# Optimization experiments

Hardware: AMD Instinct MI355X
Metric: run time of the kernel (lower is better)

Reference implementation:

```python
import jax, jax.numpy as jnp
import numpy as np

N = 5000        # n_stocks (nodes)
F = 128         # n_features
H = 4           # attention heads
C = 32          # hidden_size per head
HC = H * C      # GAT output dim = GRU input dim
GH = 256        # gru_hidden_size
E = 320000      # directed edges (before self-loops)
NEG_SLOPE = 0.2 # GATv2Conv default leaky_relu slope


def setup_inputs() -> dict:
    key = jax.random.key(0)
    ks = jax.random.split(key, 16)
    s = 0.05
    return {
        "x": jax.random.normal(ks[0], (N, F), dtype=jnp.float32),
        "edge_index": jax.random.randint(ks[1], (2, E), 0, N, dtype=jnp.int64),
        # GATv2Conv params (lin_l, lin_r with bias, attention vector, output bias)
        "W_l": jax.random.normal(ks[2], (F, HC), dtype=jnp.float32) * s,
        "b_l": jax.random.normal(ks[3], (HC,), dtype=jnp.float32) * s,
        "W_r": jax.random.normal(ks[4], (F, HC), dtype=jnp.float32) * s,
        "b_r": jax.random.normal(ks[5], (HC,), dtype=jnp.float32) * s,
        "att": jax.random.normal(ks[6], (H, C), dtype=jnp.float32) * s,
        "gat_bias": jax.random.normal(ks[7], (HC,), dtype=jnp.float32) * s,
        # GRU params (single layer, PyTorch gate order r,z,n)
        "W_ih": jax.random.normal(ks[8], (3 * GH, HC), dtype=jnp.float32) * s,
        "W_hh": jax.random.normal(ks[9], (3 * GH, GH), dtype=jnp.float32) * s,
        "b_ih": jax.random.normal(ks[10], (3 * GH,), dtype=jnp.float32) * s,
        "b_hh": jax.random.normal(ks[11], (3 * GH,), dtype=jnp.float32) * s,
        # policy head + log_std param
        "Wp": jax.random.normal(ks[12], (N, GH), dtype=jnp.float32) * s,
        "bp": jax.random.normal(ks[13], (N,), dtype=jnp.float32) * s,
        "log_std": jnp.zeros((N,), dtype=jnp.float32),
    }


def reference(x, edge_index, W_l, b_l, W_r, b_r, att, gat_bias,
              W_ih, W_hh, b_ih, b_hh, Wp, bp, log_std):
    # --- GATv2Conv (add_self_loops=True, concat heads, eval mode -> no dropout) ---
    loop = jnp.arange(N, dtype=edge_index.dtype)
    src = jnp.concatenate([edge_index[0], loop])  # message source j
    dst = jnp.concatenate([edge_index[1], loop])  # message target i

    xl = (x @ W_l + b_l).reshape(N, H, C)  # source-side transform
    xr = (x @ W_r + b_r).reshape(N, H, C)  # target-side transform

    m = xl[src] + xr[dst]                                  # [Etot, H, C]
    e = jnp.einsum('ehc,hc->eh', jax.nn.leaky_relu(m, NEG_SLOPE), att)

    # segment softmax over incoming edges per target node
    emax = jax.ops.segment_max(e, dst, num_segments=N)      # [N, H]
    ex = jnp.exp(e - emax[dst])
    denom = jax.ops.segment_sum(ex, dst, num_segments=N)    # [N, H]
    alpha = ex / denom[dst]                                 # [Etot, H]

    agg = jax.ops.segment_sum(alpha[:, :, None] * xl[src], dst, num_segments=N)
    gat_out = agg.reshape(N, HC) + gat_bias                 # [N, H*C]

    # --- GRU: each node = one batch element, seq_len=1, h0 = 0 ---
    gi = gat_out @ W_ih.T + b_ih                            # [N, 3*GH]
    gr, gz, gn = jnp.split(gi, 3, axis=1)
    hr, hz, hn = jnp.split(b_hh, 3)                          # h0=0 -> only hh bias
    r = jax.nn.sigmoid(gr + hr)
    z = jax.nn.sigmoid(gz + hz)
    n = jnp.tanh(gn + r * hn)
    h = (1.0 - z) * n                                        # [N, GH]

    # --- policy head ---
    mean = h @ Wp.T + bp                                     # [N, N]
    std = jnp.exp(jnp.clip(log_std, -10.0, 2.0))             # [N]
    return mean, std
```

## Files before the change

kernel.cpp:

```cpp
#include <hip/hip_runtime.h>
#include <hip/hip_bf16.h>
#include <float.h>

#define N_NODES 5000
#define F_IN    128
#define HC      128
#define GH      256
#define NE      320000
#define NET     325000
#define MPAD    5120
#define CAP     160
#define LIN_BLKS   313
#define DEC_BLKS  1270
#define NTHR    (DEC_BLKS * 256)

typedef __bf16 bf16;
typedef __attribute__((ext_vector_type(4))) __bf16 bf16x4;
typedef __attribute__((ext_vector_type(8))) __bf16 bf16x8;
typedef __attribute__((ext_vector_type(4))) float  f32x4;

__device__ __forceinline__ float lrelu(float v) { return v > 0.f ? v : 0.2f * v; }

__device__ __forceinline__ void gload16(const void* g, void* l) {
  __builtin_amdgcn_global_load_lds((const __attribute__((address_space(1))) void*)g,
                                   (__attribute__((address_space(3))) void*)l, 16, 0, 0);
}

__global__ void k_init(int* __restrict__ cnt) {
  int i = blockIdx.x * 256 + threadIdx.x;
  if (i < N_NODES) cnt[i] = 0;
}

#define NWIH (768 * HC)
#define NWP  (N_NODES * GH)
__global__ __launch_bounds__(256) void k_pre(
    const float* __restrict__ x,
    const float* __restrict__ Wl, const float* __restrict__ bl,
    const float* __restrict__ Wr, const float* __restrict__ br,
    bf16* __restrict__ xlb, bf16* __restrict__ xrb,
    const float* __restrict__ lstd, float* __restrict__ out_std,
    const int* __restrict__ ei, int* __restrict__ cnt, int* __restrict__ csr_s,
    const float* __restrict__ wih, const float* __restrict__ wp,
    bf16* __restrict__ wihb, bf16* __restrict__ wpb) {
  __shared__ float xs[16][F_IN];
  int t = threadIdx.x;
  if (blockIdx.x < LIN_BLKS) {
    int nb = blockIdx.x * 16;
#pragma unroll
    for (int p = 0; p < 8; ++p) {
      int idx = p * 256 + t;
      int nl = idx >> 7, c = idx & 127;
      int gn = nb + nl;
      xs[nl][c] = (gn < N_NODES) ? x[(size_t)gn * F_IN + c] : 0.f;
    }
    __syncthreads();
    int col = t & 127;
    const float* W = (t < 128) ? Wl : Wr;
    float bias = (t < 128) ? bl[col] : br[col];
    float acc[16];
#pragma unroll
    for (int m = 0; m < 16; ++m) acc[m] = bias;
#pragma unroll 4
    for (int k = 0; k < F_IN; ++k) {
      float w = W[k * HC + col];
#pragma unroll
      for (int m = 0; m < 16; ++m) acc[m] = fmaf(xs[m][k], w, acc[m]);
    }
    bf16* out = (t < 128) ? xlb : xrb;
#pragma unroll
    for (int m = 0; m < 16; ++m) {
      int gn = nb + m;
      if (gn < N_NODES) out[(size_t)gn * HC + col] = (bf16)acc[m];
    }
    if (t < 16) {
      int gn = nb + t;
      if (gn < N_NODES) out_std[gn] = expf(fminf(fmaxf(lstd[gn], -10.f), 2.f));
    }
    return;
  }
  __shared__ int mode;
  if (t == 0) {
    int f = 0;
    for (int q = 1; q < 128; q += 2) f |= ei[q];
    mode = (f == 0) ? 1 : 0;
  }
  __syncthreads();
  int e = (blockIdx.x - LIN_BLKS) * 256 + t;
  for (int i = e; i < NWIH / 4; i += NTHR) {
    float4 v = reinterpret_cast<const float4*>(wih)[i];
    bf16x4 o = {(bf16)v.x, (bf16)v.y, (bf16)v.z, (bf16)v.w};
    *reinterpret_cast<bf16x4*>(&wihb[i * 4]) = o;
  }
  for (int i = e; i < NWP / 4; i += NTHR) {
    float4 v = reinterpret_cast<const float4*>(wp)[i];
    bf16x4 o = {(bf16)v.x, (bf16)v.y, (bf16)v.z, (bf16)v.w};
    *reinterpret_cast<bf16x4*>(&wpb[i * 4]) = o;
  }
  if (e >= NET) return;
  int s, d;
  if (e >= NE) { s = d = e - NE; }
  else if (mode) { s = ei[2 * e]; d = ei[2 * (NE + e)]; }
  else           { s = ei[e];     d = ei[NE + e]; }
  int slot = atomicAdd(&cnt[d], 1);
  if (slot < CAP) csr_s[d * CAP + slot] = s;
}

__global__ __launch_bounds__(256) void k_gat(
    const bf16* __restrict__ xlb, const bf16* __restrict__ xrb,
    const int* __restrict__ csr_s, const int* __restrict__ cnt,
    const float* __restrict__ att, const float* __restrict__ gbias,
    bf16* __restrict__ gat_b) {
  int t = threadIdx.x;
  int lane = t & 63;
  int node = blockIdx.x * 4 + (t >> 6);
  if (node >= N_NODES) return;
  int c8 = lane & 15;
  int eg = lane >> 4;
  bf16x8 xr8 = *reinterpret_cast<const bf16x8*>(xrb + (size_t)node * HC + c8 * 8);
  float4 w0 = reinterpret_cast<const float4*>(att)[c8 * 2];
  float4 w1 = reinterpret_cast<const float4*>(att)[c8 * 2 + 1];
  float xr[8], wv[8];
#pragma unroll
  for (int k = 0; k < 8; ++k) xr[k] = (float)xr8[k];
  wv[0] = w0.x; wv[1] = w0.y; wv[2] = w0.z; wv[3] = w0.w;
  wv[4] = w1.x; wv[5] = w1.y; wv[6] = w1.z; wv[7] = w1.w;

  float acc[8] = {0.f, 0.f, 0.f, 0.f, 0.f, 0.f, 0.f, 0.f};
  float den = 0.f;
  int deg = cnt[node];
  deg = deg < CAP ? deg : CAP;
  int beg = node * CAP, end = node * CAP + deg;
#pragma unroll 2
  for (int p0 = beg; p0 < end; p0 += 4) {
    int p = p0 + eg;
    bool valid = p < end;
    int j = valid ? csr_s[p] : node;
    bf16x8 a8 = *reinterpret_cast<const bf16x8*>(xlb + (size_t)j * HC + c8 * 8);
    float av[8];
    float tt = 0.f;
#pragma unroll
    for (int k = 0; k < 8; ++k) {
      av[k] = (float)a8[k];
      tt = fmaf(lrelu(av[k] + xr[k]), wv[k], tt);
    }
    tt += __shfl_xor(tt, 1);
    tt += __shfl_xor(tt, 2);
    float pe = valid ? __expf(tt) : 0.f;
    den += pe;
#pragma unroll
    for (int k = 0; k < 8; ++k) acc[k] = fmaf(pe, av[k], acc[k]);
  }
#pragma unroll
  for (int m = 16; m <= 32; m <<= 1) {
    den += __shfl_xor(den, m);
#pragma unroll
    for (int k = 0; k < 8; ++k) acc[k] += __shfl_xor(acc[k], m);
  }
  if (eg == 0) {
    float4 g0 = reinterpret_cast<const float4*>(gbias)[c8 * 2];
    float4 g1 = reinterpret_cast<const float4*>(gbias)[c8 * 2 + 1];
    float gb[8] = {g0.x, g0.y, g0.z, g0.w, g1.x, g1.y, g1.z, g1.w};
    float rden = 1.f / den;
    bf16x8 o;
#pragma unroll
    for (int k = 0; k < 8; ++k) o[k] = (bf16)(acc[k] * rden + gb[k]);
    *reinterpret_cast<bf16x8*>(gat_b + (size_t)node * HC + c8 * 8) = o;
  }
}

template <bool BF16OUT>
__global__ __launch_bounds__(256) void gemm_nt_bf16(
    const bf16* __restrict__ A, const bf16* __restrict__ B,
    const float* __restrict__ bias, void* __restrict__ Cout,
    int K, int ldc, int Mstore, int Nstore, int nbx) {
  __shared__ char smem[65536];
  int t = threadIdx.x;
  int lane = t & 63, wave = t >> 6;
  int wm = wave >> 1, wn = wave & 1;
  int r16 = lane & 15, kg = lane >> 4;

  int nwg = gridDim.x;
  int cpx = nwg >> 3;
  int wg  = blockIdx.x;
  int swz = (wg & 7) * cpx + (wg >> 3);
  int bm0 = (swz % nbx) * 128;
  int bn0 = (swz / nbx) * 128;

  int rsub = lane >> 3;
  int cchk = lane & 7;

  auto STAGE = [&](int buf, int k0) {
    char* Ab = smem + buf * 32768;
#pragma unroll
    for (int q = 0; q < 4; ++q) {
      int row = (wave * 4 + q) * 8 + rsub;
      int gc = cchk ^ (row & 7);
      char* db = Ab + (wave * 4 + q) * 1024;
      gload16(&A[(size_t)(bm0 + row) * K + k0 + gc * 8], db);
      gload16(&B[(size_t)(bn0 + row) * K + k0 + gc * 8], db + 16384);
    }
  };

  f32x4 acc[4][4] = {};
  int rbA[4], rbB[4];
#pragma unroll
  for (int m = 0; m < 4; ++m) rbA[m] = (wm * 64 + m * 16 + r16) * 128;
#pragma unroll
  for (int n = 0; n < 4; ++n) rbB[n] = (wn * 64 + n * 16 + r16) * 128;
  int sw7 = r16 & 7;

  int nt = K >> 6;
  STAGE(0, 0);
  __syncthreads();
  for (int tt = 0; tt < nt; ++tt) {
    if (tt + 1 < nt) STAGE((tt & 1) ^ 1, (tt + 1) * 64);
    const char* Ab = smem + (tt & 1) * 32768;
    const char* Bb = Ab + 16384;
#pragma unroll
    for (int ks = 0; ks < 2; ++ks) {
      int ch = ((ks * 4 + kg) ^ sw7) * 16;
      bf16x8 af[4], bfr[4];
#pragma unroll
      for (int m = 0; m < 4; ++m)
        af[m] = *reinterpret_cast<const bf16x8*>(Ab + rbA[m] + ch);
#pragma unroll
      for (int n = 0; n < 4; ++n)
        bfr[n] = *reinterpret_cast<const bf16x8*>(Bb + rbB[n] + ch);
#pragma unroll
      for (int m = 0; m < 4; ++m)
#pragma unroll
        for (int n = 0; n < 4; ++n)
          acc[m][n] = __builtin_amdgcn_mfma_f32_16x16x32_bf16(af[m], bfr[n], acc[m][n], 0, 0, 0);
    }
    __syncthreads();
  }

  float bv[4];
#pragma unroll
  for (int n = 0; n < 4; ++n) {
    int gcol = bn0 + wn * 64 + n * 16 + r16;
    bv[n] = (gcol < Nstore) ? bias[gcol] : 0.f;
  }

  if constexpr (BF16OUT) {
    bf16* Cs = (bf16*)smem;
    bf16* Cg = (bf16*)Cout;
#pragma unroll
    for (int m = 0; m < 4; ++m) {
      int rb = wm * 64 + m * 16 + kg * 4;
#pragma unroll
      for (int n = 0; n < 4; ++n) {
        int cb = wn * 64 + n * 16 + r16;
#pragma unroll
        for (int r = 0; r < 4; ++r)
          Cs[(rb + r) * 128 + cb] = (bf16)(acc[m][n][r] + bv[n]);
      }
    }
    __syncthreads();
#pragma unroll
    for (int i = 0; i < 8; ++i) {
      int chunk = i * 256 + t;
      int row = chunk >> 4, c8 = chunk & 15;
      int grow = bm0 + row, gcol = bn0 + c8 * 8;
      if (grow < Mstore && gcol < Nstore)
        *reinterpret_cast<int4*>(&Cg[(size_t)grow * ldc + gcol]) =
            *reinterpret_cast<const int4*>(&Cs[row * 128 + c8 * 8]);
    }
  } else {
    float* Cs = (float*)smem;
    float* Cg = (float*)Cout;
#pragma unroll
    for (int m = 0; m < 4; ++m) {
      int rb = wm * 64 + m * 16 + kg * 4;
#pragma unroll
      for (int n = 0; n < 4; ++n) {
        int cb = wn * 64 + n * 16 + r16;
#pragma unroll
        for (int r = 0; r < 4; ++r)
          Cs[(rb + r) * 128 + cb] = acc[m][n][r] + bv[n];
      }
    }
    __syncthreads();
#pragma unroll
    for (int i = 0; i < 16; ++i) {
      int chunk = i * 256 + t;
      int row = chunk >> 5, cc = chunk & 31;
      int grow = bm0 + row, gcol = bn0 + cc * 4;
      if (grow < Mstore && gcol < Nstore) {
        f32x4 v = *reinterpret_cast<const f32x4*>(&Cs[row * 128 + cc * 4]);
        __builtin_nontemporal_store(v, reinterpret_cast<f32x4*>(&Cg[(size_t)grow * ldc + gcol]));
      }
    }
  }
}

__global__ __launch_bounds__(256) void k_gru(const bf16* __restrict__ gi,
    const float* __restrict__ bhh, bf16* __restrict__ hb) {
  int i = blockIdx.x, g = threadIdx.x;
  float gr = (float)gi[(size_t)i * 768 + g]       + bhh[g];
  float gz = (float)gi[(size_t)i * 768 + 256 + g] + bhh[256 + g];
  float gn = (float)gi[(size_t)i * 768 + 512 + g];
  float r = 1.f / (1.f + expf(-gr));
  float z = 1.f / (1.f + expf(-gz));
  float n = tanhf(gn + r * bhh[512 + g]);
  hb[(size_t)i * GH + g] = (bf16)((1.f - z) * n);
}

extern "C" void kernel_launch(void* const* d_in, const int* in_sizes, int n_in,
                              void* d_out, int out_size, void* d_ws, size_t ws_size,
                              hipStream_t stream) {
  const float* x     = (const float*)d_in[0];
  const int*   ei    = (const int*)d_in[1];
  const float* Wl    = (const float*)d_in[2];
  const float* bl    = (const float*)d_in[3];
  const float* Wr    = (const float*)d_in[4];
  const float* br    = (const float*)d_in[5];
  const float* att   = (const float*)d_in[6];
  const float* gbias = (const float*)d_in[7];
  const float* Wih   = (const float*)d_in[8];
  const float* bih   = (const float*)d_in[10];
  const float* bhh   = (const float*)d_in[11];
  const float* Wp    = (const float*)d_in[12];
  const float* bp    = (const float*)d_in[13];
  const float* lstd  = (const float*)d_in[14];
  float* out_mean = (float*)d_out;
  float* out_std  = out_mean + (size_t)N_NODES * N_NODES;

  char* w = (char*)d_ws;
  auto carve = [&](size_t bytes) {
    char* p = w; w += (bytes + 255) & ~(size_t)255; return p;
  };
  bf16*  xlb   = (bf16*)carve((size_t)N_NODES * HC * 2);
  bf16*  xrb   = (bf16*)carve((size_t)N_NODES * HC * 2);
  int*   cnt   = (int*)carve((size_t)N_NODES * 4);
  int*   csr_s = (int*)carve((size_t)N_NODES * CAP * 4);
  bf16*  gatb  = (bf16*)carve((size_t)MPAD * HC * 2);
  bf16*  wihb  = (bf16*)carve((size_t)768 * HC * 2);
  bf16*  gi    = (bf16*)carve((size_t)MPAD * 768 * 2);
  bf16*  hb    = (bf16*)carve((size_t)MPAD * GH * 2);
  bf16*  wpb   = (bf16*)carve((size_t)MPAD * GH * 2);

  k_init<<<(N_NODES + 255) / 256, 256, 0, stream>>>(cnt);
  k_pre<<<LIN_BLKS + DEC_BLKS, 256, 0, stream>>>(
      x, Wl, bl, Wr, br, xlb, xrb, lstd, out_std,
      ei, cnt, csr_s, Wih, Wp, wihb, wpb);
  k_gat<<<(N_NODES + 3) / 4, 256, 0, stream>>>(xlb, xrb, csr_s, cnt, att, gbias, gatb);
  gemm_nt_bf16<true><<<40 * 6, 256, 0, stream>>>(gatb, wihb, bih, gi, 128, 768, N_NODES, 768, 40);
  k_gru<<<N_NODES, 256, 0, stream>>>(gi, bhh, hb);
  gemm_nt_bf16<false><<<40 * 40, 256, 0, stream>>>(hb, wpb, bp, out_mean, 256, N_NODES, N_NODES, N_NODES, 40);
}
```

Measured before the change: 112.2 us.

## Fuse GRU input GEMM with GRU gate epilogue into one kernel

Replaces the separate gi GEMM (bf16 output) and elementwise GRU kernel with a single kernel. Each 64-row by 128-column tile computes the r, z and n gate accumulators for the same columns and applies sigmoid and tanh in registers before writing h. This removes the gi round trip through global memory and one launch. The cost is a 160-block grid with more accumulator registers and serialized B-tile staging, which may leave CUs underused.

```diff
diff --git a/kernel.cpp b/kernel.cpp
--- a/kernel.cpp
+++ b/kernel.cpp
@@ -20,6 +20,7 @@
 typedef __attribute__((ext_vector_type(4))) float  f32x4;
 
 __device__ __forceinline__ float lrelu(float v) { return v > 0.f ? v : 0.2f * v; }
+__device__ __forceinline__ float sigm(float v) { return 1.f / (1.f + __expf(-v)); }
 
 __device__ __forceinline__ void gload16(const void* g, void* l) {
   __builtin_amdgcn_global_load_lds((const __attribute__((address_space(1))) void*)g,
@@ -168,10 +169,110 @@
   }
 }
 
-template <bool BF16OUT>
-__global__ __launch_bounds__(256) void gemm_nt_bf16(
+__global__ __launch_bounds__(256) void k_gemm_gru(
+    const bf16* __restrict__ A, const bf16* __restrict__ wihb,
+    const float* __restrict__ bih, const float* __restrict__ bhh,
+    bf16* __restrict__ hb) {
+  __shared__ char smem[49152];
+  char* Ab = smem;
+  char* Bb = smem + 16384;
+  int t = threadIdx.x;
+  int lane = t & 63, wave = t >> 6;
+  int wm = wave >> 1, wn = wave & 1;
+  int r16 = lane & 15, kg = lane >> 4;
+  int sw7 = r16 & 7;
+  int bm = blockIdx.x >> 1, bn = blockIdx.x & 1;
+  int r0 = bm * 64, c0 = bn * 128;
+
+#pragma unroll
+  for (int q = 0; q < 4; ++q) {
+    int idx = q * 256 + t;
+    int half = idx >> 9, ih = idx & 511;
+    int row = ih >> 3, cc = ih & 7;
+    int gc = cc ^ (row & 7);
+    gload16(&A[(size_t)(r0 + row) * 128 + half * 64 + gc * 8],
+            Ab + (q * 256 + wave * 64) * 16);
+  }
+
+  auto STAGE_B = [&](int gate) {
+#pragma unroll
+    for (int q = 0; q < 8; ++q) {
+      int idx = q * 256 + t;
+      int half = idx >> 10, ih = idx & 1023;
+      int row = ih >> 3, cc = ih & 7;
+      int gc = cc ^ (row & 7);
+      gload16(&wihb[(size_t)(gate * 256 + c0 + row) * 128 + half * 64 + gc * 8],
+              Bb + (q * 256 + wave * 64) * 16);
+    }
+  };
+
+  int rowA[2], rowB[4];
+#pragma unroll
+  for (int m = 0; m < 2; ++m) rowA[m] = (wm * 32 + m * 16 + r16) * 128;
+#pragma unroll
+  for (int n = 0; n < 4; ++n) rowB[n] = (wn * 64 + n * 16 + r16) * 128;
+
+  f32x4 acc[3][2][4] = {};
+  STAGE_B(0);
+  __syncthreads();
+#pragma unroll
+  for (int g = 0; g < 3; ++g) {
+#pragma unroll
+    for (int h = 0; h < 2; ++h)
+#pragma unroll
+      for (int w = 0; w < 2; ++w) {
+        int ch = ((w * 4 + kg) ^ sw7) * 16;
+        bf16x8 af[2], bfr[4];
+#pragma unroll
+        for (int m = 0; m < 2; ++m)
+          af[m] = *reinterpret_cast<const bf16x8*>(Ab + h * 8192 + rowA[m] + ch);
+#pragma unroll
+        for (int n = 0; n < 4; ++n)
+          bfr[n] = *reinterpret_cast<const bf16x8*>(Bb + h * 16384 + rowB[n] + ch);
+#pragma unroll
+        for (int m = 0; m < 2; ++m)
+#pragma unroll
+          for (int n = 0; n < 4; ++n)
+            acc[g][m][n] = __builtin_amdgcn_mfma_f32_16x16x32_bf16(af[m], bfr[n], acc[g][m][n], 0, 0, 0);
+      }
+    __syncthreads();
+    if (g < 2) { STAGE_B(g + 1); __syncthreads(); }
+  }
+
+  bf16* hl = (bf16*)Bb;
+#pragma unroll
+  for (int n = 0; n < 4; ++n) {
+    int c = c0 + wn * 64 + n * 16 + r16;
+    float bihr = bih[c],      bhhr = bhh[c];
+    float bihz = bih[256 + c], bhhz = bhh[256 + c];
+    float bihn = bih[512 + c], bhhn = bhh[512 + c];
+#pragma unroll
+    for (int m = 0; m < 2; ++m)
+#pragma unroll
+      for (int rr = 0; rr < 4; ++rr) {
+        float rg = sigm(acc[0][m][n][rr] + bihr + bhhr);
+        float zg = sigm(acc[1][m][n][rr] + bihz + bhhz);
+        float ng = tanhf(acc[2][m][n][rr] + bihn + rg * bhhn);
+        float hv = (1.f - zg) * ng;
+        int row = wm * 32 + m * 16 + kg * 4 + rr;
+        hl[row * 128 + (wn * 64 + n * 16 + r16)] = (bf16)hv;
+      }
+  }
+  __syncthreads();
+#pragma unroll
+  for (int q = 0; q < 4; ++q) {
+    int idx = q * 256 + t;
+    int row = idx >> 4, cc = idx & 15;
+    int node = r0 + row;
+    if (node < N_NODES + 120)
+      *reinterpret_cast<int4*>(&hb[(size_t)node * GH + c0 + cc * 8]) =
+          *reinterpret_cast<const int4*>(&hl[row * 128 + cc * 8]);
+  }
+}
+
+__global__ __launch_bounds__(256) void gemm_nt_f32out(
     const bf16* __restrict__ A, const bf16* __restrict__ B,
-    const float* __restrict__ bias, void* __restrict__ Cout,
+    const float* __restrict__ bias, float* __restrict__ Cout,
     int K, int ldc, int Mstore, int Nstore, int nbx) {
   __shared__ char smem[65536];
   int t = threadIdx.x;
@@ -242,68 +343,29 @@
     bv[n] = (gcol < Nstore) ? bias[gcol] : 0.f;
   }
 
-  if constexpr (BF16OUT) {
-    bf16* Cs = (bf16*)smem;
-    bf16* Cg = (bf16*)Cout;
-#pragma unroll
-    for (int m = 0; m < 4; ++m) {
-      int rb = wm * 64 + m * 16 + kg * 4;
-#pragma unroll
-      for (int n = 0; n < 4; ++n) {
-        int cb = wn * 64 + n * 16 + r16;
-#pragma unroll
-        for (int r = 0; r < 4; ++r)
-          Cs[(rb + r) * 128 + cb] = (bf16)(acc[m][n][r] + bv[n]);
-      }
-    }
-    __syncthreads();
-#pragma unroll
-    for (int i = 0; i < 8; ++i) {
-      int chunk = i * 256 + t;
-      int row = chunk >> 4, c8 = chunk & 15;
-      int grow = bm0 + row, gcol = bn0 + c8 * 8;
-      if (grow < Mstore && gcol < Nstore)
-        *reinterpret_cast<int4*>(&Cg[(size_t)grow * ldc + gcol]) =
-            *reinterpret_cast<const int4*>(&Cs[row * 128 + c8 * 8]);
-    }
-  } else {
-    float* Cs = (float*)smem;
-    float* Cg = (float*)Cout;
-#pragma unroll
-    for (int m = 0; m < 4; ++m) {
-      int rb = wm * 64 + m * 16 + kg * 4;
-#pragma unroll
-      for (int n = 0; n < 4; ++n) {
-        int cb = wn * 64 + n * 16 + r16;
-#pragma unroll
-        for (int r = 0; r < 4; ++r)
-          Cs[(rb + r) * 128 + cb] = acc[m][n][r] + bv[n];
-      }
-    }
-    __syncthreads();
-#pragma unroll
-    for (int i = 0; i < 16; ++i) {
-      int chunk = i * 256 + t;
-      int row = chunk >> 5, cc = chunk & 31;
-      int grow = bm0 + row, gcol = bn0 + cc * 4;
-      if (grow < Mstore && gcol < Nstore) {
-        f32x4 v = *reinterpret_cast<const f32x4*>(&Cs[row * 128 + cc * 4]);
-        __builtin_nontemporal_store(v, reinterpret_cast<f32x4*>(&Cg[(size_t)grow * ldc + gcol]));
-      }
-    }
-  }
-}
-
-__global__ __launch_bounds__(256) void k_gru(const bf16* __restrict__ gi,
-    const float* __restrict__ bhh, bf16* __restrict__ hb) {
-  int i = blockIdx.x, g = threadIdx.x;
-  float gr = (float)gi[(size_t)i * 768 + g]       + bhh[g];
-  float gz = (float)gi[(size_t)i * 768 + 256 + g] + bhh[256 + g];
-  float gn = (float)gi[(size_t)i * 768 + 512 + g];
-  float r = 1.f / (1.f + expf(-gr));
-  float z = 1.f / (1.f + expf(-gz));
-  float n = tanhf(gn + r * bhh[512 + g]);
-  hb[(size_t)i * GH + g] = (bf16)((1.f - z) * n);
+  float* Cs = (float*)smem;
+#pragma unroll
+  for (int m = 0; m < 4; ++m) {
+    int rb = wm * 64 + m * 16 + kg * 4;
+#pragma unroll
+    for (int n = 0; n < 4; ++n) {
+      int cb = wn * 64 + n * 16 + r16;
+#pragma unroll
+      for (int r = 0; r < 4; ++r)
+        Cs[(rb + r) * 128 + cb] = acc[m][n][r] + bv[n];
+    }
+  }
+  __syncthreads();
+#pragma unroll
+  for (int i = 0; i < 16; ++i) {
+    int chunk = i * 256 + t;
+    int row = chunk >> 5, cc = chunk & 31;
+    int grow = bm0 + row, gcol = bn0 + cc * 4;
+    if (grow < Mstore && gcol < Nstore) {
+      f32x4 v = *reinterpret_cast<const f32x4*>(&Cs[row * 128 + cc * 4]);
+      __builtin_nontemporal_store(v, reinterpret_cast<f32x4*>(&Cout[(size_t)grow * ldc + gcol]));
+    }
+  }
 }
 
 extern "C" void kernel_launch(void* const* d_in, const int* in_sizes, int n_in,
@@ -336,7 +398,6 @@
   int*   csr_s = (int*)carve((size_t)N_NODES * CAP * 4);
   bf16*  gatb  = (bf16*)carve((size_t)MPAD * HC * 2);
   bf16*  wihb  = (bf16*)carve((size_t)768 * HC * 2);
-  bf16*  gi    = (bf16*)carve((size_t)MPAD * 768 * 2);
   bf16*  hb    = (bf16*)carve((size_t)MPAD * GH * 2);
   bf16*  wpb   = (bf16*)carve((size_t)MPAD * GH * 2);
 
@@ -345,7 +406,6 @@
       x, Wl, bl, Wr, br, xlb, xrb, lstd, out_std,
       ei, cnt, csr_s, Wih, Wp, wihb, wpb);
   k_gat<<<(N_NODES + 3) / 4, 256, 0, stream>>>(xlb, xrb, csr_s, cnt, att, gbias, gatb);
-  gemm_nt_bf16<true><<<40 * 6, 256, 0, stream>>>(gatb, wihb, bih, gi, 128, 768, N_NODES, 768, 40);
-  k_gru<<<N_NODES, 256, 0, stream>>>(gi, bhh, hb);
-  gemm_nt_bf16<false><<<40 * 40, 256, 0, stream>>>(hb, wpb, bp, out_mean, 256, N_NODES, N_NODES, N_NODES, 40);
-}
+  k_gemm_gru<<<160, 256, 0, stream>>>(gatb, wihb, bih, bhh, hb);
+  gemm_nt_f32out<<<40 * 40, 256, 0, stream>>>(hb, wpb, bp, out_mean, 256, N_NODES, N_NODES, N_NODES, 40);
+}
```

After: 112.6 us. Within noise of the previous version (+0.4%).
